# Kernel tuning notes

Hardware: AMD Instinct MI355X
Metric: run time of the kernel (lower is better)

The kernel has to match this reference:

```python
import jax, jax.numpy as jnp
import numpy as np

B, VMAX, EGO, H, ACT = 2048, 128, 15, 256, 2


def _u(k, shape, fan):
    s = 1.0 / np.sqrt(fan)
    return jax.random.uniform(k, shape, jnp.float32, -s, s)


def setup_inputs() -> dict:
    key = jax.random.key(0)
    ks = jax.random.split(key, 20)
    return {
        "state": jax.random.normal(ks[0], (B, VMAX, EGO), jnp.float32),
        "lengths": jax.random.randint(ks[1], (B,), 1, VMAX + 1),
        "Wih1": _u(ks[2], (4 * H, EGO), H), "Whh1": _u(ks[3], (4 * H, H), H),
        "bih1": _u(ks[4], (4 * H,), H), "bhh1": _u(ks[5], (4 * H,), H),
        "W1": _u(ks[6], (1024, H), H), "b1": _u(ks[7], (1024,), H),
        "W2": _u(ks[8], (1024, 1024), 1024), "b2": _u(ks[9], (1024,), 1024),
        "W3": _u(ks[10], (512, 1024), 1024), "b3": _u(ks[11], (512,), 1024),
        "W4": _u(ks[12], (256, 512), 512), "b4": _u(ks[13], (256,), 512),
        "Wih2": _u(ks[14], (4 * H, H), H), "Whh2": _u(ks[15], (4 * H, H), H),
        "bih2": _u(ks[16], (4 * H,), H), "bhh2": _u(ks[17], (4 * H,), H),
        "Wpi": _u(ks[18], (ACT, H), H), "bpi": _u(ks[19], (ACT,), H),
    }


def lstm_cell(x, h, c, Wih, Whh, bih, bhh):
    # torch.nn.LSTMCell: gates ordered i, f, g, o
    g = x @ Wih.T + bih + h @ Whh.T + bhh  # [B, 4H]
    i, f, gg, o = jnp.split(g, 4, axis=-1)
    c = jax.nn.sigmoid(f) * c + jax.nn.sigmoid(i) * jnp.tanh(gg)
    h = jax.nn.sigmoid(o) * jnp.tanh(c)
    return h, c


def reference(state, lengths, Wih1, Whh1, bih1, bhh1, W1, b1, W2, b2,
              W3, b3, W4, b4, Wih2, Whh2, bih2, bhh2, Wpi, bpi):
    Bn, V, _ = state.shape
    z = jnp.zeros((Bn, H), state.dtype)

    # Encoder: per-vehicle LSTM over ragged lengths (masked updates).
    def enc_step(carry, xs):
        h, c = carry
        x_t, t = xs
        hn, cn = lstm_cell(x_t, h, c, Wih1, Whh1, bih1, bhh1)
        m = (t < lengths)[:, None]
        return (jnp.where(m, hn, h), jnp.where(m, cn, c)), None
    (h, _), _ = jax.lax.scan(enc_step, (z, z),
                             (state.transpose(1, 0, 2), jnp.arange(V)))

    x = jax.nn.relu(h @ W1.T + b1)
    x = jax.nn.relu(x @ W2.T + b2)
    x = jax.nn.relu(x @ W3.T + b3)
    x = jax.nn.relu(x @ W4.T + b4)  # [B, 256]

    # Decoder: repeats the SAME input x each step; action = tanh(pi(cx))
    # (original applies pi to the cell state cx, kept faithful).
    def dec_step(carry, _):
        h, c = carry
        hn, cn = lstm_cell(x, h, c, Wih2, Whh2, bih2, bhh2)
        act = jnp.tanh(cn @ Wpi.T + bpi)
        return (hn, cn), act
    _, acts = jax.lax.scan(dec_step, (z, z), None, length=V)  # [V, B, ACT]
    acts = acts.transpose(1, 0, 2)  # [B, V, ACT]

    # Zero out padded timesteps (ragged output represented as padded dense).
    mask = (jnp.arange(V)[None, :] < lengths[:, None])[..., None]
    return acts * mask.astype(acts.dtype)
```

## Files before the change

### kernel.cpp

```cpp
#include <hip/hip_runtime.h>

typedef _Float16 f16;
typedef _Float16 f16x8 __attribute__((ext_vector_type(8)));
typedef float f32x4 __attribute__((ext_vector_type(4)));

#define MFMA(a,b,c) __builtin_amdgcn_mfma_f32_16x16x32_f16(a,b,c,0,0,0)

constexpr int B_ = 2048, V_ = 128, EGO_ = 15, H_ = 256;
constexpr int MT = 16;
constexpr int ENC_KT = 9;
constexpr int DEC_KT = 8;
constexpr int HSTR = 168;
constexpr int DSTR = 136;


__device__ __forceinline__ float sigf(float x){ return 1.f/(1.f+__expf(-x)); }
__device__ __forceinline__ float tanh_fast(float x){ return 1.f - 2.f/(1.f+__expf(2.f*x)); }

__device__ __forceinline__ void st_u32(uint32_t* p, uint32_t v){
    __hip_atomic_store(p, v, __ATOMIC_RELAXED, __HIP_MEMORY_SCOPE_AGENT);
}
__device__ __forceinline__ uint32_t ld_u32(const uint32_t* p){
    return __hip_atomic_load(p, __ATOMIC_RELAXED, __HIP_MEMORY_SCOPE_AGENT);
}
__device__ __forceinline__ void bypass_ld4(f16x8& d0, f16x8& d1, f16x8& d2, f16x8& d3,
                                           const f16* p0, const f16* p1,
                                           const f16* p2, const f16* p3){
    asm volatile(
        "global_load_dwordx4 %0, %4, off sc1\n\t"
        "global_load_dwordx4 %1, %5, off sc1\n\t"
        "global_load_dwordx4 %2, %6, off sc1\n\t"
        "global_load_dwordx4 %3, %7, off sc1\n\t"
        "s_waitcnt vmcnt(0)"
        : "=&v"(d0), "=&v"(d1), "=&v"(d2), "=&v"(d3)
        : "v"(p0), "v"(p1), "v"(p2), "v"(p3)
        : "memory");
}
__device__ __forceinline__ void bypass_st(f16* p, f16x8 v){
    asm volatile("global_store_dwordx4 %0, %1, off sc1" :: "v"(p), "v"(v) : "memory");
}
__device__ __forceinline__ void vm_drain(){
    asm volatile("s_waitcnt vmcnt(0)" ::: "memory");
}

__global__ void prepack_enc(const float* __restrict__ Whh1, const float* __restrict__ Wih1,
                            f16* __restrict__ dst){
    int id = blockIdx.x*256 + threadIdx.x;
    if (id >= 2*4*8*ENC_KT*64) return;
    int L = id & 63; int c = id >> 6;
    int kt = c % ENC_KT; c /= ENC_KT;
    int nt = c & 7; c >>= 3;
    int w = c & 3; int hb = c >> 2;
    int n = (nt>>1)*256 + hb*128 + w*32 + (nt&1)*16 + (L&15);
    int kb = (L>>4)*8;
    #pragma unroll
    for (int j=0;j<8;++j){
        int kin = kb + j;
        int k;
        if (kt < 4)      k = hb*128 + kt*32 + kin;
        else if (kt < 8) k = (1-hb)*128 + (kt-4)*32 + kin;
        else             k = 256 + kin;
        float x = (k < 256) ? Whh1[n*256 + k] : ((k < 271) ? Wih1[n*15 + (k-256)] : 0.f);
        dst[(size_t)id*8 + j] = (f16)x;
    }
}
__global__ void prepack_dec(const float* __restrict__ Whh2, f16* __restrict__ dst){
    int id = blockIdx.x*256 + threadIdx.x;
    if (id >= 2*4*8*DEC_KT*64) return;
    int L = id & 63; int c = id >> 6;
    int kt = c % DEC_KT; c /= DEC_KT;
    int nt = c & 7; c >>= 3;
    int w = c & 3; int hb = c >> 2;
    int n = (nt>>1)*256 + hb*128 + w*32 + (nt&1)*16 + (L&15);
    int kb = (L>>4)*8;
    #pragma unroll
    for (int j=0;j<8;++j){
        int kin = kb + j;
        int k = (kt < 4) ? (hb*128 + kt*32 + kin) : ((1-hb)*128 + (kt-4)*32 + kin);
        dst[(size_t)id*8 + j] = (f16)Whh2[n*256 + k];
    }
}
__global__ void bias_kernel(const float* bih1,const float* bhh1,const float* bih2,
                            const float* bhh2,float* be,float* bd){
    int i = blockIdx.x*256 + threadIdx.x;
    if (i < 1024){ be[i]=bih1[i]+bhh1[i]; bd[i]=bih2[i]+bhh2[i]; }
}
__global__ void convert_kernel(const float* __restrict__ src, f16* __restrict__ dst, int n){
    int i = blockIdx.x*256 + threadIdx.x;
    if (i < n) dst[i] = (f16)src[i];
}

__global__ __launch_bounds__(256,1) void encoder_kernel(
    const float* __restrict__ state, const int* __restrict__ lengths,
    const f16* __restrict__ Wp, const float* __restrict__ bias,
    f16* __restrict__ henc, f16* __restrict__ ebuf, int* __restrict__ flags)
{
    __shared__ __align__(16) f16 wlds[4*8*4*64*8];
    __shared__ __align__(16) f16 hcat[MT*HSTR];
    __shared__ int lmax_s;
    const int tid = threadIdx.x;
    const int wave = tid>>6, lane = tid&63, lr = lane&15, quad = lane>>4;
    const int bid = blockIdx.x, hb = bid>>7, g = bid&127, pbid = bid^128;
    const int row0 = g*MT;
    const int xr = tid>>4, xc = tid&15;

    for (int i=tid;i<MT*HSTR;i+=256) hcat[i] = (f16)0.f;
    if (tid < 64){
        int l = (lane<16) ? lengths[row0+lane] : 0;
        #pragma unroll
        for (int m=1;m<16;m<<=1){ int o = __shfl_xor(l, m, 64); l = (o>l)?o:l; }
        if (lane==0) lmax_s = l;
    }

    int len_r[4];
    #pragma unroll
    for (int r=0;r<4;++r) len_r[r] = lengths[row0 + quad*4 + r];

    float bias_v[8];
    #pragma unroll
    for (int nt=0;nt<8;++nt)
        bias_v[nt] = bias[(nt>>1)*256 + hb*128 + wave*32 + (nt&1)*16 + lr];

    const f16x8* Wb = (const f16x8*)Wp + (size_t)((hb*4+wave)*8*ENC_KT)*64;
    f16x8 wreg[8][5];
    #pragma unroll
    for (int nt=0;nt<8;++nt){
        #pragma unroll
        for (int kt=0;kt<4;++kt) wreg[nt][kt] = Wb[(nt*ENC_KT + kt)*64 + lane];
        wreg[nt][4] = Wb[(nt*ENC_KT + 8)*64 + lane];
    }
    f16x8* wl = (f16x8*)wlds + (size_t)wave*(8*4*64);
    #pragma unroll
    for (int nt=0;nt<8;++nt)
        #pragma unroll
        for (int p=0;p<4;++p)
            wl[(nt*4 + p)*64 + lane] = Wb[(nt*ENC_KT + 4 + p)*64 + lane];

    __syncthreads();
    const int rr = tid/15, cc = tid - rr*15;
    const size_t xbase = (size_t)(row0+rr)*V_*EGO_ + cc;
    float xreg = 0.f;
    if (tid < 240){
        hcat[rr*HSTR + 128 + cc] = (f16)state[xbase];
        xreg = state[xbase + EGO_];
    }
    float c_reg[8], h_reg[8];
    #pragma unroll
    for (int i=0;i<8;++i){ c_reg[i]=0.f; h_reg[i]=0.f; }
    __syncthreads();
    const int Lmax = lmax_s;

    for (int t=0;t<Lmax;++t){
        uint32_t f0 = (uint32_t)t;
        if (t > 0 && lane < 4) f0 = ld_u32((const uint32_t*)&flags[pbid*4 + lane]);
        f32x4 acc[8];
        #pragma unroll
        for (int nt=0;nt<8;++nt) acc[nt] = (f32x4){bias_v[nt],bias_v[nt],bias_v[nt],bias_v[nt]};
        #pragma unroll
        for (int kt=0;kt<4;++kt){
            f16x8 a = *(const f16x8*)&hcat[lr*HSTR + kt*32 + quad*8];
            #pragma unroll
            for (int nt=0;nt<8;++nt) acc[nt] = MFMA(a, wreg[nt][kt], acc[nt]);
        }
        {
            f16x8 a = *(const f16x8*)&hcat[lr*HSTR + 128 + quad*8];
            #pragma unroll
            for (int nt=0;nt<8;++nt) acc[nt] = MFMA(a, wreg[nt][4], acc[nt]);
        }
        if (t > 0){
            f16x8 b0[8];
            #pragma unroll
            for (int nt=0;nt<8;++nt) b0[nt] = wl[(nt*4 + 0)*64 + lane];
            if (lane < 4){
                while (f0 < (uint32_t)t){
                    __builtin_amdgcn_s_sleep(1);
                    f0 = ld_u32((const uint32_t*)&flags[pbid*4 + lane]);
                }
            }
            const f16* src = ebuf + ((size_t)((t-1)&1)*256 + pbid)*2048 + lr*128 + quad*8;
            f16x8 a0,a1,a2,a3;
            bypass_ld4(a0,a1,a2,a3, src, src+32, src+64, src+96);
            #pragma unroll
            for (int nt=0;nt<8;++nt) acc[nt] = MFMA(a0, b0[nt], acc[nt]);
            #pragma unroll
            for (int nt=0;nt<8;++nt) acc[nt] = MFMA(a1, wl[(nt*4+1)*64+lane], acc[nt]);
            #pragma unroll
            for (int nt=0;nt<8;++nt) acc[nt] = MFMA(a2, wl[(nt*4+2)*64+lane], acc[nt]);
            #pragma unroll
            for (int nt=0;nt<8;++nt) acc[nt] = MFMA(a3, wl[(nt*4+3)*64+lane], acc[nt]);
        }
        __syncthreads();
        #pragma unroll
        for (int s=0;s<2;++s){
            #pragma unroll
            for (int r=0;r<4;++r){
                int idx = s*4 + r;
                float gi = acc[s][r],   gf = acc[2+s][r];
                float gg = acc[4+s][r], go = acc[6+s][r];
                float cn = sigf(gf)*c_reg[idx] + sigf(gi)*tanh_fast(gg);
                float hn = sigf(go)*tanh_fast(cn);
                bool upd = (t < len_r[r]);
                c_reg[idx] = upd ? cn : c_reg[idx];
                h_reg[idx] = upd ? hn : h_reg[idx];
                hcat[(quad*4+r)*HSTR + wave*32 + s*16 + lr] = (f16)h_reg[idx];
            }
        }
        if (tid < 240) hcat[rr*HSTR + 128 + cc] = (f16)xreg;
        __syncthreads();
        {
            f16x8 h8 = *(const f16x8*)&hcat[xr*HSTR + xc*8];
            f16* dst = ebuf + ((size_t)(t&1)*256 + bid)*2048 + xr*128 + xc*8;
            bypass_st(dst, h8);
        }
        vm_drain();
        if (lane == 0) st_u32((uint32_t*)&flags[bid*4 + wave], (uint32_t)(t+1));
        if (tid < 240){
            int tn = (t+2 < V_) ? (t+2) : (V_-1);
            xreg = state[xbase + (size_t)tn*EGO_];
        }
    }
    #pragma unroll
    for (int s=0;s<2;++s)
        #pragma unroll
        for (int r=0;r<4;++r)
            henc[(size_t)(row0+quad*4+r)*H_ + hb*128 + wave*32 + s*16 + lr] = (f16)h_reg[s*4+r];
}

template<bool RELU, bool F32OUT>
__global__ __launch_bounds__(256,2) void gemm_kernel(
    const f16* __restrict__ A, const f16* __restrict__ W,
    const float* __restrict__ bias, void* __restrict__ outp,
    int M, int N, int K)
{
    constexpr int ASTR = 40;
    __shared__ __align__(16) f16 As[64*ASTR];
    __shared__ __align__(16) f16 Ws[64*ASTR];
    const int tid = threadIdx.x;
    const int wave = tid>>6, lane = tid&63, lr = lane&15, quad = lane>>4;
    const int n0 = blockIdx.x*64, m0 = blockIdx.y*64;
    const int lrow = tid>>2, lk8 = (tid&3)*8;

    f32x4 acc[4];
    #pragma unroll
    for (int mt=0;mt<4;++mt) acc[mt] = (f32x4){0.f,0.f,0.f,0.f};

    for (int k0=0;k0<K;k0+=32){
        __syncthreads();
        *(f16x8*)&As[lrow*ASTR + lk8] = *(const f16x8*)&A[(size_t)(m0+lrow)*K + k0 + lk8];
        *(f16x8*)&Ws[lrow*ASTR + lk8] = *(const f16x8*)&W[(size_t)(n0+lrow)*K + k0 + lk8];
        __syncthreads();
        f16x8 b = *(const f16x8*)&Ws[(wave*16+lr)*ASTR + quad*8];
        #pragma unroll
        for (int mt=0;mt<4;++mt){
            f16x8 a = *(const f16x8*)&As[(mt*16+lr)*ASTR + quad*8];
            acc[mt] = MFMA(a, b, acc[mt]);
        }
    }
    float bv = bias[n0 + wave*16 + lr];
    #pragma unroll
    for (int mt=0;mt<4;++mt){
        #pragma unroll
        for (int r=0;r<4;++r){
            float v = acc[mt][r] + bv;
            if (RELU) v = fmaxf(v, 0.f);
            int m = m0 + mt*16 + quad*4 + r, n = n0 + wave*16 + lr;
            if (F32OUT) ((float*)outp)[(size_t)m*N + n] = v;
            else        ((f16*)outp)[(size_t)m*N + n] = (f16)v;
        }
    }
}

__global__ __launch_bounds__(256,1) void decoder_kernel(
    const int* __restrict__ lengths, const f16* __restrict__ Wp,
    const float* __restrict__ xdec, const float* __restrict__ Wpi,
    const float* __restrict__ bpi, float* __restrict__ out,
    f16* __restrict__ ebuf, int* __restrict__ flags, float* __restrict__ pbuf)
{
    __shared__ __align__(16) f16 wlds[4*8*4*64*8];
    __shared__ __align__(16) f16 hbuf[MT*DSTR];
    __shared__ float part[4][16][2];
    __shared__ int lmax_s;
    const int tid = threadIdx.x;
    const int wave = tid>>6, lane = tid&63, lr = lane&15, quad = lane>>4;
    const int bid = blockIdx.x, hb = bid>>7, g = bid&127, pbid = bid^128;
    const int row0 = g*MT;
    const int xr = tid>>4, xc = tid&15;

    for (int i=tid;i<MT*DSTR;i+=256) hbuf[i] = (f16)0.f;
    if (tid < 64){
        int l = (lane<16) ? lengths[row0+lane] : 0;
        #pragma unroll
        for (int m=1;m<16;m<<=1){ int o = __shfl_xor(l, m, 64); l = (o>l)?o:l; }
        if (lane==0) lmax_s = l;
    }

    float xd[8][4];
    #pragma unroll
    for (int nt=0;nt<8;++nt){
        int n = (nt>>1)*256 + hb*128 + wave*32 + (nt&1)*16 + lr;
        #pragma unroll
        for (int r=0;r<4;++r) xd[nt][r] = xdec[(size_t)(row0+quad*4+r)*1024 + n];
    }
    float wpi_reg[2][2];
    #pragma unroll
    for (int a=0;a<2;++a)
        #pragma unroll
        for (int s=0;s<2;++s)
            wpi_reg[a][s] = Wpi[a*H_ + hb*128 + wave*32 + s*16 + lr];

    const f16x8* Wb = (const f16x8*)Wp + (size_t)((hb*4+wave)*8*DEC_KT)*64;
    f16x8 wreg[8][4];
    #pragma unroll
    for (int nt=0;nt<8;++nt)
        #pragma unroll
        for (int kt=0;kt<4;++kt)
            wreg[nt][kt] = Wb[(nt*DEC_KT + kt)*64 + lane];
    f16x8* wl = (f16x8*)wlds + (size_t)wave*(8*4*64);
    #pragma unroll
    for (int nt=0;nt<8;++nt)
        #pragma unroll
        for (int p=0;p<4;++p)
            wl[(nt*4 + p)*64 + lane] = Wb[(nt*DEC_KT + 4 + p)*64 + lane];

    float c_reg[8];
    #pragma unroll
    for (int i=0;i<8;++i) c_reg[i]=0.f;

    const int m_o = (tid>>1)&15, a_o = tid&1;
    const float bpi_o = bpi[a_o];
    const int len_o = (tid<32) ? lengths[row0+m_o] : 0;
    const size_t outbase = (size_t)(row0+m_o)*V_*2 + a_o;
    float own_prev = 0.f;

    __syncthreads();
    const int Lmax = lmax_s;

    for (int t=0;t<Lmax;++t){
        uint32_t f0 = (uint32_t)t;
        if (t > 0 && lane < 4) f0 = ld_u32((const uint32_t*)&flags[pbid*4 + lane]);
        f32x4 acc[8];
        #pragma unroll
        for (int nt=0;nt<8;++nt) acc[nt] = (f32x4){xd[nt][0],xd[nt][1],xd[nt][2],xd[nt][3]};
        #pragma unroll
        for (int kt=0;kt<4;++kt){
            f16x8 a = *(const f16x8*)&hbuf[lr*DSTR + kt*32 + quad*8];
            #pragma unroll
            for (int nt=0;nt<8;++nt) acc[nt] = MFMA(a, wreg[nt][kt], acc[nt]);
        }
        if (t > 0){
            f16x8 b0[8];
            #pragma unroll
            for (int nt=0;nt<8;++nt) b0[nt] = wl[(nt*4 + 0)*64 + lane];
            if (lane < 4){
                while (f0 < (uint32_t)t){
                    __builtin_amdgcn_s_sleep(1);
                    f0 = ld_u32((const uint32_t*)&flags[pbid*4 + lane]);
                }
            }
            const f16* src = ebuf + ((size_t)((t-1)&1)*256 + pbid)*2048 + lr*128 + quad*8;
            f16x8 a0,a1,a2,a3;
            bypass_ld4(a0,a1,a2,a3, src, src+32, src+64, src+96);
            #pragma unroll
            for (int nt=0;nt<8;++nt) acc[nt] = MFMA(a0, b0[nt], acc[nt]);
            #pragma unroll
            for (int nt=0;nt<8;++nt) acc[nt] = MFMA(a1, wl[(nt*4+1)*64+lane], acc[nt]);
            #pragma unroll
            for (int nt=0;nt<8;++nt) acc[nt] = MFMA(a2, wl[(nt*4+2)*64+lane], acc[nt]);
            #pragma unroll
            for (int nt=0;nt<8;++nt) acc[nt] = MFMA(a3, wl[(nt*4+3)*64+lane], acc[nt]);
            if (hb == 0 && tid < 32){
                uint32_t pu = ld_u32((const uint32_t*)pbuf + ((size_t)((t-1)&1)*128 + g)*32 + tid);
                float v = own_prev + __uint_as_float(pu) + bpi_o;
                v = tanh_fast(v);
                out[outbase + (size_t)(t-1)*2] = ((t-1) < len_o) ? v : 0.f;
            }
        }
        __syncthreads();
        float spi[4][2];
        #pragma unroll
        for (int r=0;r<4;++r){ spi[r][0]=0.f; spi[r][1]=0.f; }
        #pragma unroll
        for (int s=0;s<2;++s){
            #pragma unroll
            for (int r=0;r<4;++r){
                int idx = s*4 + r;
                float gi = acc[s][r],   gf = acc[2+s][r];
                float gg = acc[4+s][r], go = acc[6+s][r];
                float cn = sigf(gf)*c_reg[idx] + sigf(gi)*tanh_fast(gg);
                c_reg[idx] = cn;
                float hn = sigf(go)*tanh_fast(cn);
                hbuf[(quad*4+r)*DSTR + wave*32 + s*16 + lr] = (f16)hn;
                spi[r][0] += cn*wpi_reg[0][s];
                spi[r][1] += cn*wpi_reg[1][s];
            }
        }
        #pragma unroll
        for (int msk=1; msk<16; msk<<=1){
            #pragma unroll
            for (int r=0;r<4;++r){
                spi[r][0] += __shfl_xor(spi[r][0], msk, 64);
                spi[r][1] += __shfl_xor(spi[r][1], msk, 64);
            }
        }
        if (lr == 0){
            #pragma unroll
            for (int r=0;r<4;++r){
                part[wave][quad*4+r][0] = spi[r][0];
                part[wave][quad*4+r][1] = spi[r][1];
            }
        }
        __syncthreads();
        {
            f16x8 h8 = *(const f16x8*)&hbuf[xr*DSTR + xc*8];
            f16* dst = ebuf + ((size_t)(t&1)*256 + bid)*2048 + xr*128 + xc*8;
            bypass_st(dst, h8);
        }
        if (tid < 32){
            float own4 = part[0][m_o][a_o]+part[1][m_o][a_o]+part[2][m_o][a_o]+part[3][m_o][a_o];
            if (hb == 1) st_u32((uint32_t*)pbuf + ((size_t)(t&1)*128 + g)*32 + tid,
                                __float_as_uint(own4));
            else         own_prev = own4;
        }
        vm_drain();
        if (lane == 0) st_u32((uint32_t*)&flags[bid*4 + wave], (uint32_t)(t+1));
    }
    if (hb == 0 && tid < 32){
        uint32_t fv = ld_u32((const uint32_t*)&flags[pbid*4 + 0]);
        while (fv < (uint32_t)Lmax){
            __builtin_amdgcn_s_sleep(1);
            fv = ld_u32((const uint32_t*)&flags[pbid*4 + 0]);
        }
        uint32_t pu = ld_u32((const uint32_t*)pbuf + ((size_t)((Lmax-1)&1)*128 + g)*32 + tid);
        float v = own_prev + __uint_as_float(pu) + bpi_o;
        v = tanh_fast(v);
        out[outbase + (size_t)(Lmax-1)*2] = ((Lmax-1) < len_o) ? v : 0.f;
        for (int t=Lmax; t<V_; ++t) out[outbase + (size_t)t*2] = 0.f;
    }
}

extern "C" void kernel_launch(void* const* d_in, const int* in_sizes, int n_in,
                              void* d_out, int out_size, void* d_ws, size_t ws_size,
                              hipStream_t stream) {
    const float* state = (const float*)d_in[0];
    const int*   lengths=(const int*)d_in[1];
    const float* Wih1 = (const float*)d_in[2];
    const float* Whh1 = (const float*)d_in[3];
    const float* bih1 = (const float*)d_in[4];
    const float* bhh1 = (const float*)d_in[5];
    const float* W1   = (const float*)d_in[6];  const float* b1 = (const float*)d_in[7];
    const float* W2   = (const float*)d_in[8];  const float* b2 = (const float*)d_in[9];
    const float* W3   = (const float*)d_in[10]; const float* b3 = (const float*)d_in[11];
    const float* W4   = (const float*)d_in[12]; const float* b4 = (const float*)d_in[13];
    const float* Wih2 = (const float*)d_in[14]; const float* Whh2=(const float*)d_in[15];
    const float* bih2 = (const float*)d_in[16]; const float* bhh2=(const float*)d_in[17];
    const float* Wpi  = (const float*)d_in[18]; const float* bpi =(const float*)d_in[19];
    float* out = (float*)d_out;

    char* p = (char*)d_ws;
    auto alloc = [&](size_t bytes){ char* r = p; p += (bytes + 255) & ~(size_t)255; return r; };
    f16* WencP   = (f16*)alloc((size_t)2*4*8*ENC_KT*64*8*2);
    f16* WdecP   = (f16*)alloc((size_t)2*4*8*DEC_KT*64*8*2);
    f16* W1f     = (f16*)alloc((size_t)1024*256*2);
    f16* W2f     = (f16*)alloc((size_t)1024*1024*2);
    f16* W3f     = (f16*)alloc((size_t)512*1024*2);
    f16* W4f     = (f16*)alloc((size_t)256*512*2);
    f16* Wih2f   = (f16*)alloc((size_t)1024*256*2);
    float* biasE = (float*)alloc(1024*4);
    float* biasD = (float*)alloc(1024*4);
    f16* henc    = (f16*)alloc((size_t)2048*256*2);
    f16* act1    = (f16*)alloc((size_t)2048*1024*2);
    f16* act2    = (f16*)alloc((size_t)2048*1024*2);
    f16* act3    = (f16*)alloc((size_t)2048*512*2);
    f16* x4      = (f16*)alloc((size_t)2048*256*2);
    float* xdec  = (float*)alloc((size_t)2048*1024*4);
    f16* ebuf    = (f16*)alloc((size_t)2*256*2048*2);
    float* pbuf  = (float*)alloc((size_t)2*128*32*4);
    int* flags   = (int*)alloc((size_t)2048*4);

    hipMemsetAsync(flags, 0, 2048*4, stream);

    prepack_enc<<<(2*4*8*ENC_KT*64+255)/256,256,0,stream>>>(Whh1, Wih1, WencP);
    prepack_dec<<<(2*4*8*DEC_KT*64+255)/256,256,0,stream>>>(Whh2, WdecP);
    bias_kernel<<<4,256,0,stream>>>(bih1,bhh1,bih2,bhh2,biasE,biasD);
    convert_kernel<<<(1024*256+255)/256,256,0,stream>>>(W1, W1f, 1024*256);
    convert_kernel<<<(1024*1024+255)/256,256,0,stream>>>(W2, W2f, 1024*1024);
    convert_kernel<<<(512*1024+255)/256,256,0,stream>>>(W3, W3f, 512*1024);
    convert_kernel<<<(256*512+255)/256,256,0,stream>>>(W4, W4f, 256*512);
    convert_kernel<<<(1024*256+255)/256,256,0,stream>>>(Wih2, Wih2f, 1024*256);

    encoder_kernel<<<256,256,0,stream>>>(state, lengths, WencP, biasE, henc, ebuf, flags);

    gemm_kernel<true ,false><<<dim3(16,32),256,0,stream>>>(henc, W1f, b1, act1, 2048,1024,256);
    gemm_kernel<true ,false><<<dim3(16,32),256,0,stream>>>(act1, W2f, b2, act2, 2048,1024,1024);
    gemm_kernel<true ,false><<<dim3( 8,32),256,0,stream>>>(act2, W3f, b3, act3, 2048, 512,1024);
    gemm_kernel<true ,false><<<dim3( 4,32),256,0,stream>>>(act3, W4f, b4, x4,   2048, 256, 512);
    gemm_kernel<false,true ><<<dim3(16,32),256,0,stream>>>(x4, Wih2f, biasD, xdec, 2048,1024,256);

    decoder_kernel<<<256,256,0,stream>>>(lengths, WdecP, xdec, Wpi, bpi, out,
                                         ebuf, flags+1024, pbuf);
}
```

Measured before the change: 1.282 ms.

## Run decoder as one block per row tile, removing cross-block flag exchange

The decoder previously split each 16-row tile's hidden dimension across two paired blocks, which exchanged hidden-state halves and partial policy sums through global memory with spin-waited flags every timestep. Now a single block per tile computes all 1024 gate columns, keeping 3/4 of Whh2 in registers and 1/4 in LDS, with a double-buffered hidden state in shared memory. This removes inter-block polling latency and global round trips per step. In exchange each block does twice the MFMA work, and only 128 blocks are launched, so CU usage halves. The xdec preload is also packed to fp16 to save registers.

```diff
diff --git a/kernel.cpp b/kernel.cpp
--- a/kernel.cpp
+++ b/kernel.cpp
@@ -1,6 +1,7 @@
 #include <hip/hip_runtime.h>
 
 typedef _Float16 f16;
+typedef _Float16 f16x2 __attribute__((ext_vector_type(2)));
 typedef _Float16 f16x8 __attribute__((ext_vector_type(8)));
 typedef float f32x4 __attribute__((ext_vector_type(4)));
 
@@ -9,9 +10,8 @@
 constexpr int B_ = 2048, V_ = 128, EGO_ = 15, H_ = 256;
 constexpr int MT = 16;
 constexpr int ENC_KT = 9;
-constexpr int DEC_KT = 8;
 constexpr int HSTR = 168;
-constexpr int DSTR = 136;
+constexpr int DSTRD = 264;
 
 
 __device__ __forceinline__ float sigf(float x){ return 1.f/(1.f+__expf(-x)); }
@@ -66,19 +66,15 @@
 }
 __global__ void prepack_dec(const float* __restrict__ Whh2, f16* __restrict__ dst){
     int id = blockIdx.x*256 + threadIdx.x;
-    if (id >= 2*4*8*DEC_KT*64) return;
-    int L = id & 63; int c = id >> 6;
-    int kt = c % DEC_KT; c /= DEC_KT;
-    int nt = c & 7; c >>= 3;
-    int w = c & 3; int hb = c >> 2;
-    int n = (nt>>1)*256 + hb*128 + w*32 + (nt&1)*16 + (L&15);
-    int kb = (L>>4)*8;
-    #pragma unroll
-    for (int j=0;j<8;++j){
-        int kin = kb + j;
-        int k = (kt < 4) ? (hb*128 + kt*32 + kin) : ((1-hb)*128 + (kt-4)*32 + kin);
-        dst[(size_t)id*8 + j] = (f16)Whh2[n*256 + k];
-    }
+    if (id >= 512*64) return;
+    int L = id & 63; int fid = id >> 6;
+    int kt = fid & 7; int c = fid >> 3;
+    int gate = c & 3; c >>= 2;
+    int cg = c & 3; int w = c >> 2;
+    int n = gate*256 + w*64 + cg*16 + (L&15);
+    int kb = kt*32 + (L>>4)*8;
+    #pragma unroll
+    for (int j=0;j<8;++j) dst[(size_t)id*8 + j] = (f16)Whh2[n*256 + kb + j];
 }
 __global__ void bias_kernel(const float* bih1,const float* bhh1,const float* bih2,
                             const float* bhh2,float* be,float* bd){
@@ -273,125 +269,110 @@
 __global__ __launch_bounds__(256,1) void decoder_kernel(
     const int* __restrict__ lengths, const f16* __restrict__ Wp,
     const float* __restrict__ xdec, const float* __restrict__ Wpi,
-    const float* __restrict__ bpi, float* __restrict__ out,
-    f16* __restrict__ ebuf, int* __restrict__ flags, float* __restrict__ pbuf)
+    const float* __restrict__ bpi, float* __restrict__ out)
 {
-    __shared__ __align__(16) f16 wlds[4*8*4*64*8];
-    __shared__ __align__(16) f16 hbuf[MT*DSTR];
-    __shared__ float part[4][16][2];
+    __shared__ __align__(16) f16 wlds[4*32*64*8];
+    __shared__ __align__(16) f16 hbuf[2][MT*DSTRD];
+    __shared__ float part[2][4][16][2];
+    __shared__ float wpi_s[2][256];
     __shared__ int lmax_s;
     const int tid = threadIdx.x;
     const int wave = tid>>6, lane = tid&63, lr = lane&15, quad = lane>>4;
-    const int bid = blockIdx.x, hb = bid>>7, g = bid&127, pbid = bid^128;
-    const int row0 = g*MT;
-    const int xr = tid>>4, xc = tid&15;
-
-    for (int i=tid;i<MT*DSTR;i+=256) hbuf[i] = (f16)0.f;
+    const int bid = blockIdx.x;
+    const int row0 = bid*MT;
+
+    for (int i=tid;i<2*MT*DSTRD;i+=256) ((f16*)hbuf)[i] = (f16)0.f;
     if (tid < 64){
         int l = (lane<16) ? lengths[row0+lane] : 0;
         #pragma unroll
         for (int m=1;m<16;m<<=1){ int o = __shfl_xor(l, m, 64); l = (o>l)?o:l; }
         if (lane==0) lmax_s = l;
     }
-
-    float xd[8][4];
-    #pragma unroll
-    for (int nt=0;nt<8;++nt){
-        int n = (nt>>1)*256 + hb*128 + wave*32 + (nt&1)*16 + lr;
-        #pragma unroll
-        for (int r=0;r<4;++r) xd[nt][r] = xdec[(size_t)(row0+quad*4+r)*1024 + n];
-    }
-    float wpi_reg[2][2];
-    #pragma unroll
-    for (int a=0;a<2;++a)
-        #pragma unroll
-        for (int s=0;s<2;++s)
-            wpi_reg[a][s] = Wpi[a*H_ + hb*128 + wave*32 + s*16 + lr];
-
-    const f16x8* Wb = (const f16x8*)Wp + (size_t)((hb*4+wave)*8*DEC_KT)*64;
-    f16x8 wreg[8][4];
-    #pragma unroll
-    for (int nt=0;nt<8;++nt)
-        #pragma unroll
-        for (int kt=0;kt<4;++kt)
-            wreg[nt][kt] = Wb[(nt*DEC_KT + kt)*64 + lane];
-    f16x8* wl = (f16x8*)wlds + (size_t)wave*(8*4*64);
-    #pragma unroll
-    for (int nt=0;nt<8;++nt)
-        #pragma unroll
-        for (int p=0;p<4;++p)
-            wl[(nt*4 + p)*64 + lane] = Wb[(nt*DEC_KT + 4 + p)*64 + lane];
-
-    float c_reg[8];
-    #pragma unroll
-    for (int i=0;i<8;++i) c_reg[i]=0.f;
+    wpi_s[0][tid] = Wpi[tid];
+    wpi_s[1][tid] = Wpi[256 + tid];
+
+    f16x2 xd_pk[4][4][2];
+    #pragma unroll
+    for (int cg=0;cg<4;++cg)
+        #pragma unroll
+        for (int g4=0;g4<4;++g4){
+            int n = g4*256 + wave*64 + cg*16 + lr;
+            #pragma unroll
+            for (int p=0;p<2;++p){
+                float v0 = xdec[(size_t)(row0+quad*4+2*p+0)*1024 + n];
+                float v1 = xdec[(size_t)(row0+quad*4+2*p+1)*1024 + n];
+                xd_pk[cg][g4][p] = (f16x2){(f16)v0,(f16)v1};
+            }
+        }
+
+    const f16x8* Wb = (const f16x8*)Wp;
+    f16x8 wreg[4][4][6];
+    #pragma unroll
+    for (int cg=0;cg<4;++cg)
+        #pragma unroll
+        for (int g4=0;g4<4;++g4)
+            #pragma unroll
+            for (int kt=0;kt<6;++kt)
+                wreg[cg][g4][kt] = Wb[(size_t)((((wave*4+cg)*4+g4)*8)+kt)*64 + lane];
+    f16x8* wl = (f16x8*)wlds + (size_t)wave*(32*64);
+    #pragma unroll
+    for (int cg=0;cg<4;++cg)
+        #pragma unroll
+        for (int g4=0;g4<4;++g4)
+            #pragma unroll
+            for (int ktt=0;ktt<2;++ktt)
+                wl[((cg*4+g4)*2+ktt)*64 + lane] = Wb[(size_t)((((wave*4+cg)*4+g4)*8)+6+ktt)*64 + lane];
+
+    float c_reg[4][4];
+    #pragma unroll
+    for (int cg=0;cg<4;++cg)
+        #pragma unroll
+        for (int r=0;r<4;++r) c_reg[cg][r] = 0.f;
 
     const int m_o = (tid>>1)&15, a_o = tid&1;
     const float bpi_o = bpi[a_o];
     const int len_o = (tid<32) ? lengths[row0+m_o] : 0;
     const size_t outbase = (size_t)(row0+m_o)*V_*2 + a_o;
-    float own_prev = 0.f;
 
     __syncthreads();
     const int Lmax = lmax_s;
 
     for (int t=0;t<Lmax;++t){
-        uint32_t f0 = (uint32_t)t;
-        if (t > 0 && lane < 4) f0 = ld_u32((const uint32_t*)&flags[pbid*4 + lane]);
-        f32x4 acc[8];
-        #pragma unroll
-        for (int nt=0;nt<8;++nt) acc[nt] = (f32x4){xd[nt][0],xd[nt][1],xd[nt][2],xd[nt][3]};
-        #pragma unroll
-        for (int kt=0;kt<4;++kt){
-            f16x8 a = *(const f16x8*)&hbuf[lr*DSTR + kt*32 + quad*8];
-            #pragma unroll
-            for (int nt=0;nt<8;++nt) acc[nt] = MFMA(a, wreg[nt][kt], acc[nt]);
-        }
-        if (t > 0){
-            f16x8 b0[8];
-            #pragma unroll
-            for (int nt=0;nt<8;++nt) b0[nt] = wl[(nt*4 + 0)*64 + lane];
-            if (lane < 4){
-                while (f0 < (uint32_t)t){
-                    __builtin_amdgcn_s_sleep(1);
-                    f0 = ld_u32((const uint32_t*)&flags[pbid*4 + lane]);
+        const f16* hb = &hbuf[t&1][0];
+        f16* hnb = &hbuf[(t+1)&1][0];
+        float spi[4][2];
+        #pragma unroll
+        for (int r=0;r<4;++r){ spi[r][0]=0.f; spi[r][1]=0.f; }
+        #pragma unroll
+        for (int cg=0;cg<4;++cg){
+            f32x4 acc[4];
+            #pragma unroll
+            for (int g4=0;g4<4;++g4)
+                acc[g4] = (f32x4){ (float)xd_pk[cg][g4][0][0], (float)xd_pk[cg][g4][0][1],
+                                   (float)xd_pk[cg][g4][1][0], (float)xd_pk[cg][g4][1][1] };
+            #pragma unroll
+            for (int kt=0;kt<8;++kt){
+                f16x8 a = *(const f16x8*)&hb[lr*DSTRD + kt*32 + quad*8];
+                if (kt < 6){
+                    #pragma unroll
+                    for (int g4=0;g4<4;++g4) acc[g4] = MFMA(a, wreg[cg][g4][kt], acc[g4]);
+                } else {
+                    #pragma unroll
+                    for (int g4=0;g4<4;++g4)
+                        acc[g4] = MFMA(a, wl[((cg*4+g4)*2+(kt-6))*64 + lane], acc[g4]);
                 }
             }
-            const f16* src = ebuf + ((size_t)((t-1)&1)*256 + pbid)*2048 + lr*128 + quad*8;
-            f16x8 a0,a1,a2,a3;
-            bypass_ld4(a0,a1,a2,a3, src, src+32, src+64, src+96);
-            #pragma unroll
-            for (int nt=0;nt<8;++nt) acc[nt] = MFMA(a0, b0[nt], acc[nt]);
-            #pragma unroll
-            for (int nt=0;nt<8;++nt) acc[nt] = MFMA(a1, wl[(nt*4+1)*64+lane], acc[nt]);
-            #pragma unroll
-            for (int nt=0;nt<8;++nt) acc[nt] = MFMA(a2, wl[(nt*4+2)*64+lane], acc[nt]);
-            #pragma unroll
-            for (int nt=0;nt<8;++nt) acc[nt] = MFMA(a3, wl[(nt*4+3)*64+lane], acc[nt]);
-            if (hb == 0 && tid < 32){
-                uint32_t pu = ld_u32((const uint32_t*)pbuf + ((size_t)((t-1)&1)*128 + g)*32 + tid);
-                float v = own_prev + __uint_as_float(pu) + bpi_o;
-                v = tanh_fast(v);
-                out[outbase + (size_t)(t-1)*2] = ((t-1) < len_o) ? v : 0.f;
-            }
-        }
-        __syncthreads();
-        float spi[4][2];
-        #pragma unroll
-        for (int r=0;r<4;++r){ spi[r][0]=0.f; spi[r][1]=0.f; }
-        #pragma unroll
-        for (int s=0;s<2;++s){
+            const int col = wave*64 + cg*16 + lr;
+            const float w0 = wpi_s[0][col], w1 = wpi_s[1][col];
             #pragma unroll
             for (int r=0;r<4;++r){
-                int idx = s*4 + r;
-                float gi = acc[s][r],   gf = acc[2+s][r];
-                float gg = acc[4+s][r], go = acc[6+s][r];
-                float cn = sigf(gf)*c_reg[idx] + sigf(gi)*tanh_fast(gg);
-                c_reg[idx] = cn;
+                float gi = acc[0][r], gf = acc[1][r], gg = acc[2][r], go = acc[3][r];
+                float cn = sigf(gf)*c_reg[cg][r] + sigf(gi)*tanh_fast(gg);
+                c_reg[cg][r] = cn;
                 float hn = sigf(go)*tanh_fast(cn);
-                hbuf[(quad*4+r)*DSTR + wave*32 + s*16 + lr] = (f16)hn;
-                spi[r][0] += cn*wpi_reg[0][s];
-                spi[r][1] += cn*wpi_reg[1][s];
+                hnb[(quad*4+r)*DSTRD + col] = (f16)hn;
+                spi[r][0] += cn*w0;
+                spi[r][1] += cn*w1;
             }
         }
         #pragma unroll
@@ -405,37 +386,20 @@
         if (lr == 0){
             #pragma unroll
             for (int r=0;r<4;++r){
-                part[wave][quad*4+r][0] = spi[r][0];
-                part[wave][quad*4+r][1] = spi[r][1];
+                part[t&1][wave][quad*4+r][0] = spi[r][0];
+                part[t&1][wave][quad*4+r][1] = spi[r][1];
             }
         }
         __syncthreads();
-        {
-            f16x8 h8 = *(const f16x8*)&hbuf[xr*DSTR + xc*8];
-            f16* dst = ebuf + ((size_t)(t&1)*256 + bid)*2048 + xr*128 + xc*8;
-            bypass_st(dst, h8);
-        }
         if (tid < 32){
-            float own4 = part[0][m_o][a_o]+part[1][m_o][a_o]+part[2][m_o][a_o]+part[3][m_o][a_o];
-            if (hb == 1) st_u32((uint32_t*)pbuf + ((size_t)(t&1)*128 + g)*32 + tid,
-                                __float_as_uint(own4));
-            else         own_prev = own4;
-        }
-        vm_drain();
-        if (lane == 0) st_u32((uint32_t*)&flags[bid*4 + wave], (uint32_t)(t+1));
-    }
-    if (hb == 0 && tid < 32){
-        uint32_t fv = ld_u32((const uint32_t*)&flags[pbid*4 + 0]);
-        while (fv < (uint32_t)Lmax){
-            __builtin_amdgcn_s_sleep(1);
-            fv = ld_u32((const uint32_t*)&flags[pbid*4 + 0]);
-        }
-        uint32_t pu = ld_u32((const uint32_t*)pbuf + ((size_t)((Lmax-1)&1)*128 + g)*32 + tid);
-        float v = own_prev + __uint_as_float(pu) + bpi_o;
-        v = tanh_fast(v);
-        out[outbase + (size_t)(Lmax-1)*2] = ((Lmax-1) < len_o) ? v : 0.f;
+            float v = part[t&1][0][m_o][a_o] + part[t&1][1][m_o][a_o]
+                    + part[t&1][2][m_o][a_o] + part[t&1][3][m_o][a_o] + bpi_o;
+            v = tanh_fast(v);
+            out[outbase + (size_t)t*2] = (t < len_o) ? v : 0.f;
+        }
+    }
+    if (tid < 32)
         for (int t=Lmax; t<V_; ++t) out[outbase + (size_t)t*2] = 0.f;
-    }
 }
 
 extern "C" void kernel_launch(void* const* d_in, const int* in_sizes, int n_in,
@@ -459,7 +423,7 @@
     char* p = (char*)d_ws;
     auto alloc = [&](size_t bytes){ char* r = p; p += (bytes + 255) & ~(size_t)255; return r; };
     f16* WencP   = (f16*)alloc((size_t)2*4*8*ENC_KT*64*8*2);
-    f16* WdecP   = (f16*)alloc((size_t)2*4*8*DEC_KT*64*8*2);
+    f16* WdecP   = (f16*)alloc((size_t)512*64*8*2);
     f16* W1f     = (f16*)alloc((size_t)1024*256*2);
     f16* W2f     = (f16*)alloc((size_t)1024*1024*2);
     f16* W3f     = (f16*)alloc((size_t)512*1024*2);
@@ -474,13 +438,12 @@
     f16* x4      = (f16*)alloc((size_t)2048*256*2);
     float* xdec  = (float*)alloc((size_t)2048*1024*4);
     f16* ebuf    = (f16*)alloc((size_t)2*256*2048*2);
-    float* pbuf  = (float*)alloc((size_t)2*128*32*4);
     int* flags   = (int*)alloc((size_t)2048*4);
 
     hipMemsetAsync(flags, 0, 2048*4, stream);
 
     prepack_enc<<<(2*4*8*ENC_KT*64+255)/256,256,0,stream>>>(Whh1, Wih1, WencP);
-    prepack_dec<<<(2*4*8*DEC_KT*64+255)/256,256,0,stream>>>(Whh2, WdecP);
+    prepack_dec<<<128,256,0,stream>>>(Whh2, WdecP);
     bias_kernel<<<4,256,0,stream>>>(bih1,bhh1,bih2,bhh2,biasE,biasD);
     convert_kernel<<<(1024*256+255)/256,256,0,stream>>>(W1, W1f, 1024*256);
     convert_kernel<<<(1024*1024+255)/256,256,0,stream>>>(W2, W2f, 1024*1024);
@@ -496,6 +459,5 @@
     gemm_kernel<true ,false><<<dim3( 4,32),256,0,stream>>>(act3, W4f, b4, x4,   2048, 256, 512);
     gemm_kernel<false,true ><<<dim3(16,32),256,0,stream>>>(x4, Wih2f, biasD, xdec, 2048,1024,256);
 
-    decoder_kernel<<<256,256,0,stream>>>(lengths, WdecP, xdec, Wpi, bpi, out,
-                                         ebuf, flags+1024, pbuf);
-}
+    decoder_kernel<<<128,256,0,stream>>>(lengths, WdecP, xdec, Wpi, bpi, out);
+}
```

Measured after the change: 1.491 ms. 16.3% more time.

## Merge paired decoder blocks into one 512-thread block, dropping cross-block flag sync

Applied to the files above, without the earlier changes.

Before, each decoder batch tile was split across two 256-thread blocks that swapped hidden-state halves every timestep through global memory, using spin-wait flags and a partial-sum buffer. The decoder now runs as 128 blocks of 512 threads, each owning the full hidden state in shared memory, so the exchange becomes a block barrier. Recurrent weights are split across registers (3 k-tiles), LDS (2 tiles) and per-step streaming from global/L2 (3 tiles), and the xdec bias init is packed to f16 to save registers. The risks are only 128 active blocks, per-step global weight reloads, and reduced precision of the xdec contribution.

```diff
diff --git a/kernel.cpp b/kernel.cpp
--- a/kernel.cpp
+++ b/kernel.cpp
@@ -1,6 +1,7 @@
 #include <hip/hip_runtime.h>
 
 typedef _Float16 f16;
+typedef _Float16 f16x2 __attribute__((ext_vector_type(2)));
 typedef _Float16 f16x8 __attribute__((ext_vector_type(8)));
 typedef float f32x4 __attribute__((ext_vector_type(4)));
 
@@ -11,7 +12,7 @@
 constexpr int ENC_KT = 9;
 constexpr int DEC_KT = 8;
 constexpr int HSTR = 168;
-constexpr int DSTR = 136;
+constexpr int DSTR = 264;
 
 
 __device__ __forceinline__ float sigf(float x){ return 1.f/(1.f+__expf(-x)); }
@@ -72,13 +73,9 @@
     int nt = c & 7; c >>= 3;
     int w = c & 3; int hb = c >> 2;
     int n = (nt>>1)*256 + hb*128 + w*32 + (nt&1)*16 + (L&15);
-    int kb = (L>>4)*8;
-    #pragma unroll
-    for (int j=0;j<8;++j){
-        int kin = kb + j;
-        int k = (kt < 4) ? (hb*128 + kt*32 + kin) : ((1-hb)*128 + (kt-4)*32 + kin);
-        dst[(size_t)id*8 + j] = (f16)Whh2[n*256 + k];
-    }
+    int kb = kt*32 + (L>>4)*8;
+    #pragma unroll
+    for (int j=0;j<8;++j) dst[(size_t)id*8 + j] = (f16)Whh2[n*256 + kb + j];
 }
 __global__ void bias_kernel(const float* bih1,const float* bhh1,const float* bih2,
                             const float* bhh2,float* be,float* bd){
@@ -270,23 +267,21 @@
     }
 }
 
-__global__ __launch_bounds__(256,1) void decoder_kernel(
+__global__ __launch_bounds__(512,2) void decoder_kernel(
     const int* __restrict__ lengths, const f16* __restrict__ Wp,
     const float* __restrict__ xdec, const float* __restrict__ Wpi,
-    const float* __restrict__ bpi, float* __restrict__ out,
-    f16* __restrict__ ebuf, int* __restrict__ flags, float* __restrict__ pbuf)
+    const float* __restrict__ bpi, float* __restrict__ out)
 {
-    __shared__ __align__(16) f16 wlds[4*8*4*64*8];
+    __shared__ __align__(16) f16 wlds[8*16*64*8];
     __shared__ __align__(16) f16 hbuf[MT*DSTR];
-    __shared__ float part[4][16][2];
+    __shared__ float part[8][16][2];
     __shared__ int lmax_s;
     const int tid = threadIdx.x;
     const int wave = tid>>6, lane = tid&63, lr = lane&15, quad = lane>>4;
-    const int bid = blockIdx.x, hb = bid>>7, g = bid&127, pbid = bid^128;
-    const int row0 = g*MT;
-    const int xr = tid>>4, xc = tid&15;
-
-    for (int i=tid;i<MT*DSTR;i+=256) hbuf[i] = (f16)0.f;
+    const int hb = wave>>2, w3 = wave&3;
+    const int bid = blockIdx.x, row0 = bid*MT;
+
+    for (int i=tid;i<MT*DSTR;i+=512) hbuf[i] = (f16)0.f;
     if (tid < 64){
         int l = (lane<16) ? lengths[row0+lane] : 0;
         #pragma unroll
@@ -294,33 +289,37 @@
         if (lane==0) lmax_s = l;
     }
 
-    float xd[8][4];
+    f16x2 xd_pk[8][2];
     #pragma unroll
     for (int nt=0;nt<8;++nt){
-        int n = (nt>>1)*256 + hb*128 + wave*32 + (nt&1)*16 + lr;
-        #pragma unroll
-        for (int r=0;r<4;++r) xd[nt][r] = xdec[(size_t)(row0+quad*4+r)*1024 + n];
+        int n = (nt>>1)*256 + hb*128 + w3*32 + (nt&1)*16 + lr;
+        #pragma unroll
+        for (int p=0;p<2;++p){
+            float v0 = xdec[(size_t)(row0+quad*4+2*p+0)*1024 + n];
+            float v1 = xdec[(size_t)(row0+quad*4+2*p+1)*1024 + n];
+            xd_pk[nt][p] = (f16x2){(f16)v0,(f16)v1};
+        }
     }
     float wpi_reg[2][2];
     #pragma unroll
     for (int a=0;a<2;++a)
         #pragma unroll
         for (int s=0;s<2;++s)
-            wpi_reg[a][s] = Wpi[a*H_ + hb*128 + wave*32 + s*16 + lr];
-
-    const f16x8* Wb = (const f16x8*)Wp + (size_t)((hb*4+wave)*8*DEC_KT)*64;
-    f16x8 wreg[8][4];
+            wpi_reg[a][s] = Wpi[a*H_ + hb*128 + w3*32 + s*16 + lr];
+
+    const f16x8* Wb = (const f16x8*)Wp + (size_t)((hb*4+w3)*8*DEC_KT)*64;
+    f16x8 wreg[8][3];
     #pragma unroll
     for (int nt=0;nt<8;++nt)
         #pragma unroll
-        for (int kt=0;kt<4;++kt)
+        for (int kt=0;kt<3;++kt)
             wreg[nt][kt] = Wb[(nt*DEC_KT + kt)*64 + lane];
-    f16x8* wl = (f16x8*)wlds + (size_t)wave*(8*4*64);
+    f16x8* wl = (f16x8*)wlds + (size_t)wave*(8*2*64);
     #pragma unroll
     for (int nt=0;nt<8;++nt)
         #pragma unroll
-        for (int p=0;p<4;++p)
-            wl[(nt*4 + p)*64 + lane] = Wb[(nt*DEC_KT + 4 + p)*64 + lane];
+        for (int kk=0;kk<2;++kk)
+            wl[(nt*2 + kk)*64 + lane] = Wb[(nt*DEC_KT + 3 + kk)*64 + lane];
 
     float c_reg[8];
     #pragma unroll
@@ -330,49 +329,38 @@
     const float bpi_o = bpi[a_o];
     const int len_o = (tid<32) ? lengths[row0+m_o] : 0;
     const size_t outbase = (size_t)(row0+m_o)*V_*2 + a_o;
-    float own_prev = 0.f;
 
     __syncthreads();
     const int Lmax = lmax_s;
 
     for (int t=0;t<Lmax;++t){
-        uint32_t f0 = (uint32_t)t;
-        if (t > 0 && lane < 4) f0 = ld_u32((const uint32_t*)&flags[pbid*4 + lane]);
+        f16x8 wc[8];
+        #pragma unroll
+        for (int nt=0;nt<8;++nt) wc[nt] = Wb[(nt*DEC_KT + 5)*64 + lane];
         f32x4 acc[8];
         #pragma unroll
-        for (int nt=0;nt<8;++nt) acc[nt] = (f32x4){xd[nt][0],xd[nt][1],xd[nt][2],xd[nt][3]};
-        #pragma unroll
-        for (int kt=0;kt<4;++kt){
+        for (int nt=0;nt<8;++nt)
+            acc[nt] = (f32x4){ (float)xd_pk[nt][0][0], (float)xd_pk[nt][0][1],
+                               (float)xd_pk[nt][1][0], (float)xd_pk[nt][1][1] };
+        #pragma unroll
+        for (int kt=0;kt<3;++kt){
             f16x8 a = *(const f16x8*)&hbuf[lr*DSTR + kt*32 + quad*8];
             #pragma unroll
             for (int nt=0;nt<8;++nt) acc[nt] = MFMA(a, wreg[nt][kt], acc[nt]);
         }
-        if (t > 0){
-            f16x8 b0[8];
-            #pragma unroll
-            for (int nt=0;nt<8;++nt) b0[nt] = wl[(nt*4 + 0)*64 + lane];
-            if (lane < 4){
-                while (f0 < (uint32_t)t){
-                    __builtin_amdgcn_s_sleep(1);
-                    f0 = ld_u32((const uint32_t*)&flags[pbid*4 + lane]);
-                }
-            }
-            const f16* src = ebuf + ((size_t)((t-1)&1)*256 + pbid)*2048 + lr*128 + quad*8;
-            f16x8 a0,a1,a2,a3;
-            bypass_ld4(a0,a1,a2,a3, src, src+32, src+64, src+96);
-            #pragma unroll
-            for (int nt=0;nt<8;++nt) acc[nt] = MFMA(a0, b0[nt], acc[nt]);
-            #pragma unroll
-            for (int nt=0;nt<8;++nt) acc[nt] = MFMA(a1, wl[(nt*4+1)*64+lane], acc[nt]);
-            #pragma unroll
-            for (int nt=0;nt<8;++nt) acc[nt] = MFMA(a2, wl[(nt*4+2)*64+lane], acc[nt]);
-            #pragma unroll
-            for (int nt=0;nt<8;++nt) acc[nt] = MFMA(a3, wl[(nt*4+3)*64+lane], acc[nt]);
-            if (hb == 0 && tid < 32){
-                uint32_t pu = ld_u32((const uint32_t*)pbuf + ((size_t)((t-1)&1)*128 + g)*32 + tid);
-                float v = own_prev + __uint_as_float(pu) + bpi_o;
-                v = tanh_fast(v);
-                out[outbase + (size_t)(t-1)*2] = ((t-1) < len_o) ? v : 0.f;
+        #pragma unroll
+        for (int kt=3;kt<5;++kt){
+            f16x8 a = *(const f16x8*)&hbuf[lr*DSTR + kt*32 + quad*8];
+            #pragma unroll
+            for (int nt=0;nt<8;++nt) acc[nt] = MFMA(a, wl[(nt*2 + (kt-3))*64 + lane], acc[nt]);
+        }
+        #pragma unroll
+        for (int ktc=5;ktc<8;++ktc){
+            f16x8 a = *(const f16x8*)&hbuf[lr*DSTR + ktc*32 + quad*8];
+            #pragma unroll
+            for (int nt=0;nt<8;++nt){
+                acc[nt] = MFMA(a, wc[nt], acc[nt]);
+                if (ktc < 7) wc[nt] = Wb[(nt*DEC_KT + ktc + 1)*64 + lane];
             }
         }
         __syncthreads();
@@ -389,7 +377,7 @@
                 float cn = sigf(gf)*c_reg[idx] + sigf(gi)*tanh_fast(gg);
                 c_reg[idx] = cn;
                 float hn = sigf(go)*tanh_fast(cn);
-                hbuf[(quad*4+r)*DSTR + wave*32 + s*16 + lr] = (f16)hn;
+                hbuf[(quad*4+r)*DSTR + hb*128 + w3*32 + s*16 + lr] = (f16)hn;
                 spi[r][0] += cn*wpi_reg[0][s];
                 spi[r][1] += cn*wpi_reg[1][s];
             }
@@ -410,32 +398,16 @@
             }
         }
         __syncthreads();
-        {
-            f16x8 h8 = *(const f16x8*)&hbuf[xr*DSTR + xc*8];
-            f16* dst = ebuf + ((size_t)(t&1)*256 + bid)*2048 + xr*128 + xc*8;
-            bypass_st(dst, h8);
-        }
         if (tid < 32){
-            float own4 = part[0][m_o][a_o]+part[1][m_o][a_o]+part[2][m_o][a_o]+part[3][m_o][a_o];
-            if (hb == 1) st_u32((uint32_t*)pbuf + ((size_t)(t&1)*128 + g)*32 + tid,
-                                __float_as_uint(own4));
-            else         own_prev = own4;
-        }
-        vm_drain();
-        if (lane == 0) st_u32((uint32_t*)&flags[bid*4 + wave], (uint32_t)(t+1));
-    }
-    if (hb == 0 && tid < 32){
-        uint32_t fv = ld_u32((const uint32_t*)&flags[pbid*4 + 0]);
-        while (fv < (uint32_t)Lmax){
-            __builtin_amdgcn_s_sleep(1);
-            fv = ld_u32((const uint32_t*)&flags[pbid*4 + 0]);
-        }
-        uint32_t pu = ld_u32((const uint32_t*)pbuf + ((size_t)((Lmax-1)&1)*128 + g)*32 + tid);
-        float v = own_prev + __uint_as_float(pu) + bpi_o;
-        v = tanh_fast(v);
-        out[outbase + (size_t)(Lmax-1)*2] = ((Lmax-1) < len_o) ? v : 0.f;
+            float v = bpi_o;
+            #pragma unroll
+            for (int w=0;w<8;++w) v += part[w][m_o][a_o];
+            v = tanh_fast(v);
+            out[outbase + (size_t)t*2] = (t < len_o) ? v : 0.f;
+        }
+    }
+    if (tid < 32)
         for (int t=Lmax; t<V_; ++t) out[outbase + (size_t)t*2] = 0.f;
-    }
 }
 
 extern "C" void kernel_launch(void* const* d_in, const int* in_sizes, int n_in,
@@ -474,10 +446,9 @@
     f16* x4      = (f16*)alloc((size_t)2048*256*2);
     float* xdec  = (float*)alloc((size_t)2048*1024*4);
     f16* ebuf    = (f16*)alloc((size_t)2*256*2048*2);
-    float* pbuf  = (float*)alloc((size_t)2*128*32*4);
-    int* flags   = (int*)alloc((size_t)2048*4);
-
-    hipMemsetAsync(flags, 0, 2048*4, stream);
+    int* flags   = (int*)alloc((size_t)1024*4);
+
+    hipMemsetAsync(flags, 0, 1024*4, stream);
 
     prepack_enc<<<(2*4*8*ENC_KT*64+255)/256,256,0,stream>>>(Whh1, Wih1, WencP);
     prepack_dec<<<(2*4*8*DEC_KT*64+255)/256,256,0,stream>>>(Whh2, WdecP);
@@ -496,6 +467,5 @@
     gemm_kernel<true ,false><<<dim3( 4,32),256,0,stream>>>(act3, W4f, b4, x4,   2048, 256, 512);
     gemm_kernel<false,true ><<<dim3(16,32),256,0,stream>>>(x4, Wih2f, biasD, xdec, 2048,1024,256);
 
-    decoder_kernel<<<256,256,0,stream>>>(lengths, WdecP, xdec, Wpi, bpi, out,
-                                         ebuf, flags+1024, pbuf);
-}
+    decoder_kernel<<<128,512,0,stream>>>(lengths, WdecP, xdec, Wpi, bpi, out);
+}
```

After: 1.532 ms. +19.5%, slower.
